# Kernel tuning notes

Measured on AMD Instinct MI355X. Metric: run time of the kernel, lower is better.

## Reference

```python
import jax, jax.numpy as jnp
import numpy as np

B, T, C = 4, 2048, 1024
H = 16
D = C // H  # 64


def setup_inputs() -> dict:
    key = jax.random.key(0)
    ks = jax.random.split(key, 4)
    s = 0.02
    return {
        "x": jax.random.normal(ks[0], (B, T, C), dtype=jnp.float32),
        "w_qkv": jax.random.normal(ks[1], (C, 3 * C), dtype=jnp.float32) * s,
        "b_qkv": jnp.zeros((3 * C,), dtype=jnp.float32),
        "w_proj": jax.random.normal(ks[2], (C, C), dtype=jnp.float32) * s,
        "b_proj": jnp.zeros((C,), dtype=jnp.float32),
    }


def reference(x, w_qkv, b_qkv, w_proj, b_proj):
    Bx, Tx, Cx = x.shape
    qkv = x @ w_qkv + b_qkv                     # [B,T,3C]
    q, k, v = jnp.split(qkv, 3, axis=-1)
    # [B,T,C] -> [B,H,T,D]
    def heads(t):
        return t.reshape(Bx, Tx, H, D).transpose(0, 2, 1, 3)
    q, k, v = heads(q), heads(k), heads(v)
    scale = 1.0 / jnp.sqrt(jnp.float32(D))
    att = jnp.einsum("bhqd,bhkd->bhqk", q, k) * scale
    causal = jnp.tril(jnp.ones((Tx, Tx), dtype=bool))
    att = jnp.where(causal[None, None], att, -jnp.inf)
    att = jax.nn.softmax(att, axis=-1)
    y = jnp.einsum("bhqk,bhkd->bhqd", att, v)   # [B,H,T,D]
    y = y.transpose(0, 2, 1, 3).reshape(Bx, Tx, Cx)
    return y @ w_proj + b_proj
```

## Files before the change

kernel.cpp:

```cpp
#include <hip/hip_runtime.h>
#include <hip/hip_bf16.h>
#include <cstdint>
#include <cstddef>

#define BB 4
#define TT 2048
#define CC 1024
#define HH 16
#define DD 64
#define MM (BB*TT)

typedef short bf16x8 __attribute__((ext_vector_type(8)));
typedef float f32x4 __attribute__((ext_vector_type(4)));

typedef const __attribute__((address_space(1))) void GV;
typedef __attribute__((address_space(3))) void LV;
#define GLL16(g, l) __builtin_amdgcn_global_load_lds((GV*)(g), (LV*)(l), 16, 0, 0)

__device__ __forceinline__ short f2b(float f) {
  __hip_bfloat16 h = __float2bfloat16(f);
  return *reinterpret_cast<short*>(&h);
}

__global__ void cvt_kernel(const float* __restrict__ in, short* __restrict__ out, int n4) {
  int i = blockIdx.x * blockDim.x + threadIdx.x;
  if (i < n4) {
    float4 v = ((const float4*)in)[i];
    short4 o;
    o.x = f2b(v.x); o.y = f2b(v.y); o.z = f2b(v.z); o.w = f2b(v.w);
    ((short4*)out)[i] = o;
  }
}

__global__ void transpose_cvt(const float* __restrict__ in, short* __restrict__ out,
                              int K, int N) {
  __shared__ short t[32][33];
  int n0 = blockIdx.x * 32, k0 = blockIdx.y * 32;
  int tx = threadIdx.x, ty = threadIdx.y;
  #pragma unroll
  for (int r = ty; r < 32; r += 8)
    t[r][tx] = f2b(in[(size_t)(k0 + r) * N + n0 + tx]);
  __syncthreads();
  #pragma unroll
  for (int r = ty; r < 32; r += 8)
    out[(size_t)(n0 + r) * K + k0 + tx] = t[tx][r];
}

template<int EPI>
__global__ __launch_bounds__(256)
void gemm_bf16(const short* __restrict__ A, const short* __restrict__ Bt,
               const float* __restrict__ bias, int M, int N, int K,
               short* __restrict__ Qb, short* __restrict__ Kb, short* __restrict__ Vt,
               float* __restrict__ Cout)
{
  constexpr int BK = 32;
  __shared__ short As[128 * BK];
  __shared__ short Bs[128 * BK];
  const int tid = threadIdx.x;
  const int lane = tid & 63, wave = tid >> 6;
  const int g = lane >> 4, qq = lane & 15;
  const int gx = gridDim.x;
  int flat = blockIdx.y * gx + blockIdx.x;
  int cpx = (gx * gridDim.y) >> 3;
  int swz = (flat & 7) * cpx + (flat >> 3);
  const int m0 = (swz / gx) * 128, n0 = (swz % gx) * 128;
  const int wr = wave >> 1, wc = wave & 1;

  f32x4 acc[4][4] = {};
  for (int k0 = 0; k0 < K; k0 += BK) {
    __syncthreads();
    #pragma unroll
    for (int i = 0; i < 2; ++i) {
      int id = i * 256 + tid; int row = id >> 2, off = id & 3;
      GLL16(A + (size_t)(m0 + row) * K + k0 + off * 8, As + id * 8);
    }
    #pragma unroll
    for (int i = 0; i < 2; ++i) {
      int id = i * 256 + tid; int row = id >> 2, off = id & 3;
      GLL16(Bt + (size_t)(n0 + row) * K + k0 + off * 8, Bs + id * 8);
    }
    __syncthreads();
    bf16x8 af[4], bfr[4];
    #pragma unroll
    for (int mi = 0; mi < 4; ++mi)
      af[mi] = *(const bf16x8*)(As + (wr * 64 + mi * 16 + qq) * BK + g * 8);
    #pragma unroll
    for (int ni = 0; ni < 4; ++ni)
      bfr[ni] = *(const bf16x8*)(Bs + (wc * 64 + ni * 16 + qq) * BK + g * 8);
    #pragma unroll
    for (int mi = 0; mi < 4; ++mi)
      #pragma unroll
      for (int ni = 0; ni < 4; ++ni)
        acc[mi][ni] = __builtin_amdgcn_mfma_f32_16x16x32_bf16(af[mi], bfr[ni], acc[mi][ni], 0, 0, 0);
  }

  const int brow = m0 + wr * 64, bcol = n0 + wc * 64;
  #pragma unroll
  for (int ni = 0; ni < 4; ++ni) {
    int n = bcol + ni * 16 + qq;
    float bs = bias[n];
    if (EPI == 0) {
      int sec = n >> 10, cc = n & 1023, h = cc >> 6, d = cc & 63;
      float qscale = (sec == 0) ? 0.125f : 1.0f;
      #pragma unroll
      for (int mi = 0; mi < 4; ++mi) {
        int t0 = brow + mi * 16 + g * 4;
        int b = t0 >> 11, tt = t0 & 2047;
        if (sec == 2) {
          size_t base = ((size_t)(b * HH + h) * DD + d) * TT + tt;
          short4 o;
          o.x = f2b(acc[mi][ni][0] + bs); o.y = f2b(acc[mi][ni][1] + bs);
          o.z = f2b(acc[mi][ni][2] + bs); o.w = f2b(acc[mi][ni][3] + bs);
          *(short4*)(Vt + base) = o;
        } else {
          short* dst = (sec == 0) ? Qb : Kb;
          size_t base = ((size_t)(b * HH + h) * TT + tt) * DD + d;
          #pragma unroll
          for (int r = 0; r < 4; ++r)
            dst[base + (size_t)r * DD] = f2b((acc[mi][ni][r] + bs) * qscale);
        }
      }
    } else {
      #pragma unroll
      for (int mi = 0; mi < 4; ++mi) {
        int t0 = brow + mi * 16 + g * 4;
        #pragma unroll
        for (int r = 0; r < 4; ++r)
          Cout[(size_t)(t0 + r) * N + n] = acc[mi][ni][r] + bs;
      }
    }
  }
}

__global__ __launch_bounds__(256, 2)
void attn_kernel(const short* __restrict__ Qb, const short* __restrict__ Kb,
                 const short* __restrict__ Vt, short* __restrict__ Yout)
{
  __shared__ short Kbuf[2][64 * 64];
  __shared__ short Vbuf[2][64 * 64];
  __shared__ short Plds[4][16 * 64];
  const int bid = blockIdx.x;
  const int bh = bid & 63;
  const int qt = 15 - (bid >> 6);
  const int tid = threadIdx.x, w = tid >> 6, lane = tid & 63;
  const int g = lane >> 4, qq = lane & 15;
  const size_t headQK = (size_t)bh * TT * DD;
  const size_t headV  = (size_t)bh * DD * TT;
  const int q0 = qt * 128;
  const int nt = 2 * qt + 2;
  const int sw = (qq & 7) << 4;
  const float FIXM = 6.0f;

#define STAGE(bufi, kv0_) do {                                                   \
    int id0 = tid; int row0 = id0 >> 3;                                          \
    int so0 = ((((id0 & 7) * 16) ^ ((row0 & 7) << 4)) >> 1);                     \
    GLL16(Kb + headQK + (size_t)((kv0_) + row0) * DD + so0, &Kbuf[bufi][0] + id0 * 8); \
    GLL16(Vt + headV + (size_t)row0 * TT + (kv0_) + so0, &Vbuf[bufi][0] + id0 * 8);    \
    int id1 = 256 + tid; int row1 = id1 >> 3;                                    \
    int so1 = ((((id1 & 7) * 16) ^ ((row1 & 7) << 4)) >> 1);                     \
    GLL16(Kb + headQK + (size_t)((kv0_) + row1) * DD + so1, &Kbuf[bufi][0] + id1 * 8); \
    GLL16(Vt + headV + (size_t)row1 * TT + (kv0_) + so1, &Vbuf[bufi][0] + id1 * 8);    \
  } while (0)

  bf16x8 qf[2][2];
  #pragma unroll
  for (int qt2 = 0; qt2 < 2; ++qt2) {
    int qrow = q0 + qt2 * 64 + w * 16 + qq;
    qf[qt2][0] = *(const bf16x8*)(Qb + headQK + (size_t)qrow * DD + g * 8);
    qf[qt2][1] = *(const bf16x8*)(Qb + headQK + (size_t)qrow * DD + 32 + g * 8);
  }

  f32x4 yacc[2][4] = {};
  float l_run[2] = { 0.f, 0.f };
  char* pb = (char*)&Plds[w][0];

  STAGE(0, 0);

  for (int kt = 0; kt < nt; ++kt) {
    const int p = kt & 1;
    const int kv0 = kt * 64;
    if (kt + 1 < nt) {
      STAGE(p ^ 1, kv0 + 64);
      asm volatile("s_waitcnt vmcnt(4)" ::: "memory");
    } else {
      asm volatile("s_waitcnt vmcnt(0)" ::: "memory");
    }
    __builtin_amdgcn_s_barrier();
    __builtin_amdgcn_sched_barrier(0);

    const char* kbase = (const char*)&Kbuf[p][0];
    const char* vbase = (const char*)&Vbuf[p][0];
    const bool skip0 = (kv0 > q0 + w * 16 + 15);

    f32x4 sa[2][4] = {};
    __builtin_amdgcn_s_setprio(1);
    #pragma unroll
    for (int kb = 0; kb < 4; ++kb) {
      int lrow = kb * 16 + qq;
      bf16x8 kf0 = *(const bf16x8*)(kbase + lrow * 128 + ((g * 16) ^ sw));
      bf16x8 kf1 = *(const bf16x8*)(kbase + lrow * 128 + ((64 + g * 16) ^ sw));
      if (!skip0) {
        sa[0][kb] = __builtin_amdgcn_mfma_f32_16x16x32_bf16(kf0, qf[0][0], sa[0][kb], 0, 0, 0);
        sa[0][kb] = __builtin_amdgcn_mfma_f32_16x16x32_bf16(kf1, qf[0][1], sa[0][kb], 0, 0, 0);
      }
      sa[1][kb] = __builtin_amdgcn_mfma_f32_16x16x32_bf16(kf0, qf[1][0], sa[1][kb], 0, 0, 0);
      sa[1][kb] = __builtin_amdgcn_mfma_f32_16x16x32_bf16(kf1, qf[1][1], sa[1][kb], 0, 0, 0);
    }
    __builtin_amdgcn_s_setprio(0);

    bf16x8 vf[4][2];
    #pragma unroll
    for (int db = 0; db < 4; ++db) {
      int lrow = db * 16 + qq;
      vf[db][0] = *(const bf16x8*)(vbase + lrow * 128 + ((g * 16) ^ sw));
      vf[db][1] = *(const bf16x8*)(vbase + lrow * 128 + ((64 + g * 16) ^ sw));
    }

    #pragma unroll
    for (int qt2 = 0; qt2 < 2; ++qt2) {
      if (qt2 == 0 && skip0) continue;
      const int qsb = q0 + qt2 * 64 + w * 16;
      const bool need_mask = (kv0 + 63 > qsb);
      const int qcol = qsb + qq;

      float p16[16]; float ls = 0.f;
      #pragma unroll
      for (int kb = 0; kb < 4; ++kb)
        #pragma unroll
        for (int r = 0; r < 4; ++r) {
          float v = sa[qt2][kb][r];
          if (need_mask) {
            int key = kv0 + kb * 16 + g * 4 + r;
            if (key > qcol) v = -INFINITY;
          }
          float e = __expf(v - FIXM);
          p16[kb * 4 + r] = e;
          ls += e;
        }
      l_run[qt2] += ls;

      #pragma unroll
      for (int kb = 0; kb < 4; ++kb) {
        short4 o;
        o.x = f2b(p16[kb * 4 + 0]); o.y = f2b(p16[kb * 4 + 1]);
        o.z = f2b(p16[kb * 4 + 2]); o.w = f2b(p16[kb * 4 + 3]);
        int wb = qq * 128 + ((kb * 32 + g * 8) ^ sw);
        *(short4*)(pb + wb) = o;
      }

      __builtin_amdgcn_s_setprio(1);
      #pragma unroll
      for (int kk = 0; kk < 2; ++kk) {
        int rb = qq * 128 + ((kk * 64 + g * 16) ^ sw);
        bf16x8 pf = *(const bf16x8*)(pb + rb);
        #pragma unroll
        for (int db = 0; db < 4; ++db)
          yacc[qt2][db] = __builtin_amdgcn_mfma_f32_16x16x32_bf16(pf, vf[db][kk], yacc[qt2][db], 0, 0, 0);
      }
      __builtin_amdgcn_s_setprio(0);
    }

    __builtin_amdgcn_sched_barrier(0);
    __builtin_amdgcn_s_barrier();
  }
#undef STAGE

  const int b = bh >> 4, h = bh & 15;
  #pragma unroll
  for (int qt2 = 0; qt2 < 2; ++qt2) {
    float lt = l_run[qt2];
    lt += __shfl_xor(lt, 16);
    lt += __shfl_xor(lt, 32);
    float li[4];
    #pragma unroll
    for (int r = 0; r < 4; ++r) li[r] = 1.f / __shfl(lt, g * 4 + r);
    #pragma unroll
    for (int db = 0; db < 4; ++db)
      #pragma unroll
      for (int r = 0; r < 4; ++r) {
        int t = q0 + qt2 * 64 + w * 16 + g * 4 + r;
        Yout[((size_t)(b * TT + t)) * CC + h * DD + db * 16 + qq] = f2b(yacc[qt2][db][r] * li[r]);
      }
  }
}

extern "C" void kernel_launch(void* const* d_in, const int* in_sizes, int n_in,
                              void* d_out, int out_size, void* d_ws, size_t ws_size,
                              hipStream_t stream)
{
  const float* x      = (const float*)d_in[0];
  const float* w_qkv  = (const float*)d_in[1];
  const float* b_qkv  = (const float*)d_in[2];
  const float* w_proj = (const float*)d_in[3];
  const float* b_proj = (const float*)d_in[4];
  float* out = (float*)d_out;

  short* ws     = (short*)d_ws;
  short* xb     = ws;
  short* wqkvT  = ws + 8388608;
  short* wprojT = ws + 11534336;
  short* Qb     = ws + 12582912;
  short* Kb     = ws + 20971520;
  short* Vt     = ws + 29360128;

  hipLaunchKernelGGL(cvt_kernel, dim3(8192), dim3(256), 0, stream, x, xb, 2097152);
  hipLaunchKernelGGL(transpose_cvt, dim3(96, 32), dim3(32, 8), 0, stream, w_qkv, wqkvT, 1024, 3072);
  hipLaunchKernelGGL(transpose_cvt, dim3(32, 32), dim3(32, 8), 0, stream, w_proj, wprojT, 1024, 1024);
  hipLaunchKernelGGL((gemm_bf16<0>), dim3(24, 64), dim3(256), 0, stream,
                     xb, wqkvT, b_qkv, MM, 3 * CC, CC, Qb, Kb, Vt, (float*)nullptr);
  hipLaunchKernelGGL(attn_kernel, dim3(1024), dim3(256), 0, stream, Qb, Kb, Vt, xb);
  hipLaunchKernelGGL((gemm_bf16<1>), dim3(8, 64), dim3(256), 0, stream,
                     xb, wprojT, b_proj, MM, CC, CC, (short*)nullptr, (short*)nullptr, (short*)nullptr, out);
}
```

Baseline: 188.9 us.

## Use 256x256 tiled QKV GEMM with 4-stage async LDS pipeline

Replaces the generic 128x128 QKV projection GEMM with a dedicated 512-thread kernel that computes 256x256 output tiles, uses global_load_lds with a 4-deep ring buffer of 32-wide K slices, and XOR-swizzles LDS addresses to avoid bank conflicts. Explicit vmcnt waits, barriers and setprio around the MFMA block are meant to overlap global loads with matrix math and raise arithmetic intensity per loaded byte. The projection GEMM is split out as a non-templated kernel. The larger tile yields only 384 blocks, and heavy register and LDS use (128KB LDS per block) limits occupancy.

```diff
diff --git a/kernel.cpp b/kernel.cpp
--- a/kernel.cpp
+++ b/kernel.cpp
@@ -46,11 +46,108 @@
     out[(size_t)(n0 + r) * K + k0 + tx] = t[tx][r];
 }
 
-template<int EPI>
+__global__ __launch_bounds__(512, 2)
+void gemm_qkv256(const short* __restrict__ A, const short* __restrict__ Bt,
+                 const float* __restrict__ bias,
+                 short* __restrict__ Qb, short* __restrict__ Kb, short* __restrict__ Vt)
+{
+  __shared__ short Abuf[4][256 * 32];
+  __shared__ short Bbuf[4][256 * 32];
+  const int tid = threadIdx.x;
+  const int w = tid >> 6, lane = tid & 63;
+  const int g = lane >> 4, qq = lane & 15;
+  const int wr = w >> 2, wc = w & 3;
+  const int gx = gridDim.x;
+  int flat = blockIdx.y * gx + blockIdx.x;
+  int cpx = (gx * gridDim.y) >> 3;
+  int swz = (flat & 7) * cpx + (flat >> 3);
+  const int m0 = (swz / gx) * 256, n0 = (swz % gx) * 256;
+
+  const int r0 = tid >> 2, c0 = tid & 3;
+  const int sc = (c0 * 8) ^ ((r0 & 6) << 2);
+  const size_t aoff0 = (size_t)(m0 + r0) * 1024 + sc;
+  const size_t aoff1 = (size_t)(m0 + r0 + 128) * 1024 + sc;
+  const size_t boff0 = (size_t)(n0 + r0) * 1024 + sc;
+  const size_t boff1 = (size_t)(n0 + r0 + 128) * 1024 + sc;
+  char* ABb = (char*)&Abuf[0][0];
+  char* BBb = (char*)&Bbuf[0][0];
+  const int ldst = tid * 16;
+
+#define STG(b, kt) do {                                              \
+    GLL16(A + aoff0 + (kt) * 32, ABb + (b) * 16384 + ldst);          \
+    GLL16(A + aoff1 + (kt) * 32, ABb + (b) * 16384 + 8192 + ldst);   \
+    GLL16(Bt + boff0 + (kt) * 32, BBb + (b) * 16384 + ldst);         \
+    GLL16(Bt + boff1 + (kt) * 32, BBb + (b) * 16384 + 8192 + ldst);  \
+  } while (0)
+
+  f32x4 acc[8][4] = {};
+  STG(0, 0); STG(1, 1); STG(2, 2); STG(3, 3);
+
+  const int rsw = (g * 16) ^ ((qq & 6) << 3);
+  for (int t = 0; t < 32; ++t) {
+    if (t <= 28)      asm volatile("s_waitcnt vmcnt(12)" ::: "memory");
+    else if (t == 29) asm volatile("s_waitcnt vmcnt(8)" ::: "memory");
+    else if (t == 30) asm volatile("s_waitcnt vmcnt(4)" ::: "memory");
+    else              asm volatile("s_waitcnt vmcnt(0)" ::: "memory");
+    __builtin_amdgcn_s_barrier();
+    __builtin_amdgcn_sched_barrier(0);
+
+    const char* ab = ABb + (t & 3) * 16384;
+    const char* bb = BBb + (t & 3) * 16384;
+    bf16x8 af[8], bf[4];
+    #pragma unroll
+    for (int mi = 0; mi < 8; ++mi)
+      af[mi] = *(const bf16x8*)(ab + (wr * 128 + mi * 16 + qq) * 64 + rsw);
+    #pragma unroll
+    for (int ni = 0; ni < 4; ++ni)
+      bf[ni] = *(const bf16x8*)(bb + (wc * 64 + ni * 16 + qq) * 64 + rsw);
+
+    __builtin_amdgcn_s_setprio(1);
+    #pragma unroll
+    for (int mi = 0; mi < 8; ++mi)
+      #pragma unroll
+      for (int ni = 0; ni < 4; ++ni)
+        acc[mi][ni] = __builtin_amdgcn_mfma_f32_16x16x32_bf16(af[mi], bf[ni], acc[mi][ni], 0, 0, 0);
+    __builtin_amdgcn_s_setprio(0);
+
+    __builtin_amdgcn_sched_barrier(0);
+    __builtin_amdgcn_s_barrier();
+    __builtin_amdgcn_sched_barrier(0);
+    if (t + 4 < 32) STG(t & 3, t + 4);
+  }
+#undef STG
+
+  const int brow = m0 + wr * 128, bcol = n0 + wc * 64;
+  #pragma unroll
+  for (int ni = 0; ni < 4; ++ni) {
+    int n = bcol + ni * 16 + qq;
+    float bs = bias[n];
+    int sec = n >> 10, cc = n & 1023, h = cc >> 6, d = cc & 63;
+    float qscale = (sec == 0) ? 0.125f : 1.0f;
+    #pragma unroll
+    for (int mi = 0; mi < 8; ++mi) {
+      int t0 = brow + mi * 16 + g * 4;
+      int b = t0 >> 11, tt = t0 & 2047;
+      if (sec == 2) {
+        size_t base = ((size_t)(b * HH + h) * DD + d) * TT + tt;
+        short4 o;
+        o.x = f2b(acc[mi][ni][0] + bs); o.y = f2b(acc[mi][ni][1] + bs);
+        o.z = f2b(acc[mi][ni][2] + bs); o.w = f2b(acc[mi][ni][3] + bs);
+        *(short4*)(Vt + base) = o;
+      } else {
+        short* dst = (sec == 0) ? Qb : Kb;
+        size_t base = ((size_t)(b * HH + h) * TT + tt) * DD + d;
+        #pragma unroll
+        for (int r = 0; r < 4; ++r)
+          dst[base + (size_t)r * DD] = f2b((acc[mi][ni][r] + bs) * qscale);
+      }
+    }
+  }
+}
+
 __global__ __launch_bounds__(256)
-void gemm_bf16(const short* __restrict__ A, const short* __restrict__ Bt,
+void gemm_proj(const short* __restrict__ A, const short* __restrict__ Bt,
                const float* __restrict__ bias, int M, int N, int K,
-               short* __restrict__ Qb, short* __restrict__ Kb, short* __restrict__ Vt,
                float* __restrict__ Cout)
 {
   constexpr int BK = 32;
@@ -99,35 +196,12 @@
   for (int ni = 0; ni < 4; ++ni) {
     int n = bcol + ni * 16 + qq;
     float bs = bias[n];
-    if (EPI == 0) {
-      int sec = n >> 10, cc = n & 1023, h = cc >> 6, d = cc & 63;
-      float qscale = (sec == 0) ? 0.125f : 1.0f;
-      #pragma unroll
-      for (int mi = 0; mi < 4; ++mi) {
-        int t0 = brow + mi * 16 + g * 4;
-        int b = t0 >> 11, tt = t0 & 2047;
-        if (sec == 2) {
-          size_t base = ((size_t)(b * HH + h) * DD + d) * TT + tt;
-          short4 o;
-          o.x = f2b(acc[mi][ni][0] + bs); o.y = f2b(acc[mi][ni][1] + bs);
-          o.z = f2b(acc[mi][ni][2] + bs); o.w = f2b(acc[mi][ni][3] + bs);
-          *(short4*)(Vt + base) = o;
-        } else {
-          short* dst = (sec == 0) ? Qb : Kb;
-          size_t base = ((size_t)(b * HH + h) * TT + tt) * DD + d;
-          #pragma unroll
-          for (int r = 0; r < 4; ++r)
-            dst[base + (size_t)r * DD] = f2b((acc[mi][ni][r] + bs) * qscale);
-        }
-      }
-    } else {
-      #pragma unroll
-      for (int mi = 0; mi < 4; ++mi) {
-        int t0 = brow + mi * 16 + g * 4;
-        #pragma unroll
-        for (int r = 0; r < 4; ++r)
-          Cout[(size_t)(t0 + r) * N + n] = acc[mi][ni][r] + bs;
-      }
+    #pragma unroll
+    for (int mi = 0; mi < 4; ++mi) {
+      int t0 = brow + mi * 16 + g * 4;
+      #pragma unroll
+      for (int r = 0; r < 4; ++r)
+        Cout[(size_t)(t0 + r) * N + n] = acc[mi][ni][r] + bs;
     }
   }
 }
@@ -306,9 +380,9 @@
   hipLaunchKernelGGL(cvt_kernel, dim3(8192), dim3(256), 0, stream, x, xb, 2097152);
   hipLaunchKernelGGL(transpose_cvt, dim3(96, 32), dim3(32, 8), 0, stream, w_qkv, wqkvT, 1024, 3072);
   hipLaunchKernelGGL(transpose_cvt, dim3(32, 32), dim3(32, 8), 0, stream, w_proj, wprojT, 1024, 1024);
-  hipLaunchKernelGGL((gemm_bf16<0>), dim3(24, 64), dim3(256), 0, stream,
-                     xb, wqkvT, b_qkv, MM, 3 * CC, CC, Qb, Kb, Vt, (float*)nullptr);
+  hipLaunchKernelGGL(gemm_qkv256, dim3(12, 32), dim3(512), 0, stream,
+                     xb, wqkvT, b_qkv, Qb, Kb, Vt);
   hipLaunchKernelGGL(attn_kernel, dim3(1024), dim3(256), 0, stream, Qb, Kb, Vt, xb);
-  hipLaunchKernelGGL((gemm_bf16<1>), dim3(8, 64), dim3(256), 0, stream,
-                     xb, wprojT, b_proj, MM, CC, CC, (short*)nullptr, (short*)nullptr, (short*)nullptr, out);
-}
+  hipLaunchKernelGGL(gemm_proj, dim3(8, 64), dim3(256), 0, stream,
+                     xb, wprojT, b_proj, MM, CC, CC, out);
+}
```

New measurement: 199.4 us. 1.06x slower.

## Double-buffer GEMM LDS tiles with async prefetch and XOR-swizzled layout

Applied to the files above, without the earlier changes.

Rewrites the bf16 GEMM main loop to double-buffer the A and B shared-memory tiles. The next K-tile is issued through global_load_lds before waiting on the current one (vmcnt(4)), so global loads overlap the MFMA work. It also applies an XOR swizzle to the LDS column offsets to reduce bank conflicts on fragment reads, and raises wave priority during the MFMA block. This doubles LDS use per block, which may lower occupancy, and depends on correct manual waitcnt and barrier placement.

```diff
diff --git a/kernel.cpp b/kernel.cpp
--- a/kernel.cpp
+++ b/kernel.cpp
@@ -48,14 +48,13 @@
 
 template<int EPI>
 __global__ __launch_bounds__(256)
-void gemm_bf16(const short* __restrict__ A, const short* __restrict__ Bt,
-               const float* __restrict__ bias, int M, int N, int K,
-               short* __restrict__ Qb, short* __restrict__ Kb, short* __restrict__ Vt,
-               float* __restrict__ Cout)
+void gemm128(const short* __restrict__ A, const short* __restrict__ Bt,
+             const float* __restrict__ bias, int M, int N, int K,
+             short* __restrict__ Qb, short* __restrict__ Kb, short* __restrict__ Vt,
+             float* __restrict__ Cout)
 {
-  constexpr int BK = 32;
-  __shared__ short As[128 * BK];
-  __shared__ short Bs[128 * BK];
+  __shared__ short As[2][128 * 32];
+  __shared__ short Bs[2][128 * 32];
   const int tid = threadIdx.x;
   const int lane = tid & 63, wave = tid >> 6;
   const int g = lane >> 4, qq = lane & 15;
@@ -66,33 +65,63 @@
   const int m0 = (swz / gx) * 128, n0 = (swz % gx) * 128;
   const int wr = wave >> 1, wc = wave & 1;
 
+  const int r0a = tid >> 2, c0 = tid & 3;
+  const int sca = (c0 * 8) ^ ((r0a & 6) << 2);
+  const int r1a = (256 + tid) >> 2;
+  const int sca1 = (c0 * 8) ^ ((r1a & 6) << 2);
+  const size_t aoff0 = (size_t)(m0 + r0a) * K + sca;
+  const size_t aoff1 = (size_t)(m0 + r1a) * K + sca1;
+  const size_t boff0 = (size_t)(n0 + r0a) * K + sca;
+  const size_t boff1 = (size_t)(n0 + r1a) * K + sca1;
+  const int ld0 = tid * 16, ld1 = (256 + tid) * 16;
+  char* ABb = (char*)&As[0][0];
+  char* BBb = (char*)&Bs[0][0];
+
+#define STG(b, k0_) do {                                   \
+    GLL16(A + aoff0 + (k0_), ABb + (b) * 8192 + ld0);      \
+    GLL16(A + aoff1 + (k0_), ABb + (b) * 8192 + ld1);      \
+    GLL16(Bt + boff0 + (k0_), BBb + (b) * 8192 + ld0);     \
+    GLL16(Bt + boff1 + (k0_), BBb + (b) * 8192 + ld1);     \
+  } while (0)
+
+  const int rsw = (g * 16) ^ ((qq & 6) << 3);
+  const int NT = K >> 5;
   f32x4 acc[4][4] = {};
-  for (int k0 = 0; k0 < K; k0 += BK) {
-    __syncthreads();
-    #pragma unroll
-    for (int i = 0; i < 2; ++i) {
-      int id = i * 256 + tid; int row = id >> 2, off = id & 3;
-      GLL16(A + (size_t)(m0 + row) * K + k0 + off * 8, As + id * 8);
-    }
-    #pragma unroll
-    for (int i = 0; i < 2; ++i) {
-      int id = i * 256 + tid; int row = id >> 2, off = id & 3;
-      GLL16(Bt + (size_t)(n0 + row) * K + k0 + off * 8, Bs + id * 8);
-    }
-    __syncthreads();
+
+  STG(0, 0);
+  for (int t = 0; t < NT; ++t) {
+    const int p = t & 1;
+    if (t + 1 < NT) {
+      STG(p ^ 1, (t + 1) * 32);
+      asm volatile("s_waitcnt vmcnt(4)" ::: "memory");
+    } else {
+      asm volatile("s_waitcnt vmcnt(0)" ::: "memory");
+    }
+    __builtin_amdgcn_s_barrier();
+    __builtin_amdgcn_sched_barrier(0);
+
+    const char* ab = ABb + p * 8192;
+    const char* bb = BBb + p * 8192;
     bf16x8 af[4], bfr[4];
     #pragma unroll
     for (int mi = 0; mi < 4; ++mi)
-      af[mi] = *(const bf16x8*)(As + (wr * 64 + mi * 16 + qq) * BK + g * 8);
+      af[mi] = *(const bf16x8*)(ab + (wr * 64 + mi * 16 + qq) * 64 + rsw);
     #pragma unroll
     for (int ni = 0; ni < 4; ++ni)
-      bfr[ni] = *(const bf16x8*)(Bs + (wc * 64 + ni * 16 + qq) * BK + g * 8);
+      bfr[ni] = *(const bf16x8*)(bb + (wc * 64 + ni * 16 + qq) * 64 + rsw);
+
+    __builtin_amdgcn_s_setprio(1);
     #pragma unroll
     for (int mi = 0; mi < 4; ++mi)
       #pragma unroll
       for (int ni = 0; ni < 4; ++ni)
         acc[mi][ni] = __builtin_amdgcn_mfma_f32_16x16x32_bf16(af[mi], bfr[ni], acc[mi][ni], 0, 0, 0);
-  }
+    __builtin_amdgcn_s_setprio(0);
+
+    __builtin_amdgcn_sched_barrier(0);
+    __builtin_amdgcn_s_barrier();
+  }
+#undef STG
 
   const int brow = m0 + wr * 64, bcol = n0 + wc * 64;
   #pragma unroll
@@ -306,9 +335,9 @@
   hipLaunchKernelGGL(cvt_kernel, dim3(8192), dim3(256), 0, stream, x, xb, 2097152);
   hipLaunchKernelGGL(transpose_cvt, dim3(96, 32), dim3(32, 8), 0, stream, w_qkv, wqkvT, 1024, 3072);
   hipLaunchKernelGGL(transpose_cvt, dim3(32, 32), dim3(32, 8), 0, stream, w_proj, wprojT, 1024, 1024);
-  hipLaunchKernelGGL((gemm_bf16<0>), dim3(24, 64), dim3(256), 0, stream,
+  hipLaunchKernelGGL((gemm128<0>), dim3(24, 64), dim3(256), 0, stream,
                      xb, wqkvT, b_qkv, MM, 3 * CC, CC, Qb, Kb, Vt, (float*)nullptr);
   hipLaunchKernelGGL(attn_kernel, dim3(1024), dim3(256), 0, stream, Qb, Kb, Vt, xb);
-  hipLaunchKernelGGL((gemm_bf16<1>), dim3(8, 64), dim3(256), 0, stream,
+  hipLaunchKernelGGL((gemm128<1>), dim3(8, 64), dim3(256), 0, stream,
                      xb, wprojT, b_proj, MM, CC, CC, (short*)nullptr, (short*)nullptr, (short*)nullptr, out);
 }
```

Result: faster. 178.0 us, median of 3 (-5.8%).
